# Kernel optimization log

Measured on AMD Instinct MI355X. Metric: run time of the kernel, lower is better.

Reference implementation:

```python
import jax, jax.numpy as jnp
import numpy as np

IN_FEATURES, OUT_FEATURES, KERNEL_DIMS = 1024, 128, 8
BATCH = 256


def setup_inputs() -> dict:
    key = jax.random.key(0)
    kx, kT = jax.random.split(key)
    x = jax.random.normal(kx, (BATCH, IN_FEATURES), dtype=jnp.float32)
    T = jax.random.normal(kT, (IN_FEATURES, OUT_FEATURES, KERNEL_DIMS), dtype=jnp.float32)
    return {"x": x, "T": T}


def reference(x, T):
    B = x.shape[0]
    in_f, out_f, kd = T.shape
    # M: (B, out_features, kernel_dims)
    M = (x @ T.reshape(in_f, out_f * kd)).reshape(B, out_f, kd)
    # pairwise L1 distance over kernel dims: (B, B, out_features)
    diffs = jnp.abs(M[None, :, :, :] - M[:, None, :, :]).sum(axis=3)
    # similarity features: sum over other samples, subtract self-term (exp(0)=1)
    c = jnp.exp(-diffs).sum(axis=1) - 1.0  # (B, out_features)
    return jnp.concatenate([x, c], axis=1)
```

## Files before the change

### kernel.cpp

```cpp
#include <hip/hip_runtime.h>
#include <stdint.h>

#define BATCH 256
#define INF   1024
#define OUTF  128
#define KD    8
#define NN    1024
#define OROW  1152

#define XCHW 2048
#define TCHW 2112

typedef __attribute__((ext_vector_type(8))) short short8;
typedef __attribute__((ext_vector_type(4))) float f32x4;

__device__ __forceinline__ unsigned short f2bf(float f) {
    union { float f; uint32_t u; } v; v.f = f;
    uint32_t r = v.u + 0x7FFFu + ((v.u >> 16) & 1u);
    return (unsigned short)(r >> 16);
}

__device__ __forceinline__ void stage_xt(
    const float* __restrict__ x, const float* __restrict__ T,
    float* xbuf, float* tbuf, int a0, int n0, int c, int wave, int lane)
{
    {
        const int r = lane >> 4, seg = lane & 15;
        #pragma unroll
        for (int p = 0; p < 2; ++p) {
            const int i = wave * 2 + p;
            const int row = i * 4 + r;
            const int segS = seg ^ (row & 7);
            const float* src = x + (size_t)(a0 + row) * INF + c * 64 + segS * 4;
            float* dst = xbuf + i * 256;
            __builtin_amdgcn_global_load_lds(
                (const __attribute__((address_space(1))) unsigned int*)src,
                (__attribute__((address_space(3))) unsigned int*)dst, 16, 0, 0);
        }
    }
    {
        const int kr = lane >> 3, seg = lane & 7;
        #pragma unroll
        for (int p = 0; p < 2; ++p) {
            const int i = wave * 2 + p;
            const int k = i * 8 + kr;
            const float* src = T + (size_t)(c * 64 + k) * NN + n0 + seg * 4;
            float* dst = tbuf + i * 264;
            __builtin_amdgcn_global_load_lds(
                (const __attribute__((address_space(1))) unsigned int*)src,
                (__attribute__((address_space(3))) unsigned int*)dst, 16, 0, 0);
        }
    }
}

__global__ __launch_bounds__(256, 2) void gemm_kernel(
    const float* __restrict__ x, const float* __restrict__ T,
    float* __restrict__ out)
{
    __shared__ __align__(16) float xls[3 * XCHW];
    __shared__ __align__(16) float tls[3 * TCHW];

    const int bid = blockIdx.x;
    const int a0 = (bid & 7) << 5;
    const int n0 = (bid >> 3) << 5;
    const int t = threadIdx.x, wave = t >> 6, lane = t & 63;
    const int rc = lane & 15, quad = lane >> 4;
    const int h = wave >> 1, g = wave & 1;
    const int rloc = h * 16 + rc;
    const int r7 = rc & 7;
    const int cn = g * 16 + rc;

    stage_xt(x, T, xls, tls, a0, n0, 0, wave, lane);
    stage_xt(x, T, xls + XCHW, tls + TCHW, a0, n0, 1, wave, lane);

    f32x4 acc = {0.f, 0.f, 0.f, 0.f};

    for (int c = 0; c < 16; ++c) {
        if (c == 15) { asm volatile("s_waitcnt vmcnt(0)" ::: "memory"); }
        else         { asm volatile("s_waitcnt vmcnt(4)" ::: "memory"); }
        __builtin_amdgcn_sched_barrier(0);
        __builtin_amdgcn_s_barrier();
        if (c + 2 < 16)
            stage_xt(x, T, xls + ((c + 2) % 3) * XCHW, tls + ((c + 2) % 3) * TCHW,
                     a0, n0, c + 2, wave, lane);
        const float* xc = xls + (c % 3) * XCHW;
        const float* tc = tls + (c % 3) * TCHW;
        #pragma unroll
        for (int ks = 0; ks < 2; ++ks) {
            f32x4 av0 = *(const f32x4*)(xc + rloc * 64 + (((ks * 8 + quad * 2 + 0) ^ r7) << 2));
            f32x4 av1 = *(const f32x4*)(xc + rloc * 64 + (((ks * 8 + quad * 2 + 1) ^ r7) << 2));
            float bv[8];
            #pragma unroll
            for (int j = 0; j < 8; ++j)
                bv[j] = tc[(ks * 4 + quad) * 264 + j * 32 + cn];
            short8 af, bf;
            af[0] = (short)f2bf(av0[0]); af[1] = (short)f2bf(av0[1]);
            af[2] = (short)f2bf(av0[2]); af[3] = (short)f2bf(av0[3]);
            af[4] = (short)f2bf(av1[0]); af[5] = (short)f2bf(av1[1]);
            af[6] = (short)f2bf(av1[2]); af[7] = (short)f2bf(av1[3]);
            #pragma unroll
            for (int j = 0; j < 8; ++j) bf[j] = (short)f2bf(bv[j]);
            acc = __builtin_amdgcn_mfma_f32_16x16x32_bf16(af, bf, acc, 0, 0, 0);
        }
    }

    #pragma unroll
    for (int r = 0; r < 4; ++r)
        out[(size_t)(a0 + h * 16 + quad * 4 + r) * OROW + (n0 + g * 16 + rc)] = acc[r];
}

__global__ __launch_bounds__(256, 4) void pair_kernel(
    const float* __restrict__ Msrc, float* __restrict__ out)
{
    __shared__ __align__(16) float Mloc[256 * 12];
    __shared__ float red[256];
    const int o = blockIdx.x >> 1;
    const int ha = blockIdx.x & 1;
    const int t = threadIdx.x;

    {
        const float* src = Msrc + (size_t)t * OROW + o * 8;
        f32x4 v0 = *(const f32x4*)(src);
        f32x4 v1 = *(const f32x4*)(src + 4);
        *(f32x4*)(Mloc + t * 12) = v0;
        *(f32x4*)(Mloc + t * 12 + 4) = v1;
    }
    __syncthreads();

    const int ai = t & 127, hb = t >> 7;
    const int a = ha * 128 + ai;
    f32x4 m0 = *(const f32x4*)(Mloc + a * 12);
    f32x4 m1 = *(const f32x4*)(Mloc + a * 12 + 4);
    float ssum = 0.f;
    #pragma unroll 4
    for (int j = 0; j < 128; ++j) {
        const float* mb = Mloc + (hb * 128 + j) * 12;
        f32x4 q0 = *(const f32x4*)(mb);
        f32x4 q1 = *(const f32x4*)(mb + 4);
        float d = fabsf(m0[0] - q0[0]) + fabsf(m0[1] - q0[1])
                + fabsf(m0[2] - q0[2]) + fabsf(m0[3] - q0[3])
                + fabsf(m1[0] - q1[0]) + fabsf(m1[1] - q1[1])
                + fabsf(m1[2] - q1[2]) + fabsf(m1[3] - q1[3]);
        ssum += __expf(-d);
    }
    red[t] = ssum;
    __syncthreads();
    if (t < 128)
        out[(size_t)(ha * 128 + t) * OROW + INF + o] = red[t] + red[t + 128] - 1.0f;
}

__global__ __launch_bounds__(256) void copy_kernel(
    const float* __restrict__ x, float* __restrict__ out)
{
    const int bx = blockIdx.x, t = threadIdx.x;
    #pragma unroll
    for (int p = 0; p < 4; ++p) {
        const int a = bx * 4 + p;
        const int j = t * 4;
        float4 v = *(const float4*)(x + (size_t)a * INF + j);
        *(float4*)(out + (size_t)a * OROW + j) = v;
    }
}

extern "C" void kernel_launch(void* const* d_in, const int* in_sizes, int n_in,
                              void* d_out, int out_size, void* d_ws, size_t ws_size,
                              hipStream_t stream) {
    const float* x = (const float*)d_in[0];
    const float* T = (const float*)d_in[1];
    float* out = (float*)d_out;
    (void)d_ws; (void)ws_size;

    gemm_kernel<<<256, 256, 0, stream>>>(x, T, out);
    pair_kernel<<<256, 256, 0, stream>>>(out, out);
    copy_kernel<<<64, 256, 0, stream>>>(x, out);
}
```

Before: 85.95 us.

## Deepen GEMM LDS pipeline, fuse copy into pair kernel, use workspace for M

The GEMM now uses a six-buffer LDS ring with five chunks in flight. Its inner step is written in inline asm that issues LDS reads and then a single lgkmcnt wait, uses hardware packed bf16 conversion, and splits the work across two accumulators. M goes to a separate workspace buffer, so the x copy no longer has to wait for the pair kernel, and the copy kernel is merged into the pair kernel, removing one launch. The pair kernel moves to 512 threads, splitting the inner loop four ways, and loads M into LDS with direct global-to-LDS loads. The risks are more LDS per block, which lowers occupancy, and hand-written waitcnt values that must match the number of loads in flight.

```diff
diff --git a/kernel.cpp b/kernel.cpp
--- a/kernel.cpp
+++ b/kernel.cpp
@@ -4,47 +4,56 @@
 #define BATCH 256
 #define INF   1024
 #define OUTF  128
-#define KD    8
 #define NN    1024
 #define OROW  1152
 
-#define XCHW 2048
-#define TCHW 2112
+#define XCH   2048
+#define TCH   2112
+#define NBUF  6
 
 typedef __attribute__((ext_vector_type(8))) short short8;
 typedef __attribute__((ext_vector_type(4))) float f32x4;
 
-__device__ __forceinline__ unsigned short f2bf(float f) {
-    union { float f; uint32_t u; } v; v.f = f;
-    uint32_t r = v.u + 0x7FFFu + ((v.u >> 16) & 1u);
-    return (unsigned short)(r >> 16);
+__device__ __forceinline__ short8 cvt8v(f32x4 lo, f32x4 hi) {
+    union { short8 s; uint32_t u[4]; } r;
+    asm("v_cvt_pk_bf16_f32 %0, %1, %2" : "=v"(r.u[0]) : "v"(lo[0]), "v"(lo[1]));
+    asm("v_cvt_pk_bf16_f32 %0, %1, %2" : "=v"(r.u[1]) : "v"(lo[2]), "v"(lo[3]));
+    asm("v_cvt_pk_bf16_f32 %0, %1, %2" : "=v"(r.u[2]) : "v"(hi[0]), "v"(hi[1]));
+    asm("v_cvt_pk_bf16_f32 %0, %1, %2" : "=v"(r.u[3]) : "v"(hi[2]), "v"(hi[3]));
+    return r.s;
+}
+__device__ __forceinline__ short8 cvt8s(float a, float b, float c, float d,
+                                        float e, float f, float g, float h) {
+    union { short8 s; uint32_t u[4]; } r;
+    asm("v_cvt_pk_bf16_f32 %0, %1, %2" : "=v"(r.u[0]) : "v"(a), "v"(b));
+    asm("v_cvt_pk_bf16_f32 %0, %1, %2" : "=v"(r.u[1]) : "v"(c), "v"(d));
+    asm("v_cvt_pk_bf16_f32 %0, %1, %2" : "=v"(r.u[2]) : "v"(e), "v"(f));
+    asm("v_cvt_pk_bf16_f32 %0, %1, %2" : "=v"(r.u[3]) : "v"(g), "v"(h));
+    return r.s;
 }
 
 __device__ __forceinline__ void stage_xt(
     const float* __restrict__ x, const float* __restrict__ T,
     float* xbuf, float* tbuf, int a0, int n0, int c, int wave, int lane)
 {
-    {
-        const int r = lane >> 4, seg = lane & 15;
+    {   const int r = lane >> 4, seg = lane & 15;
         #pragma unroll
         for (int p = 0; p < 2; ++p) {
             const int i = wave * 2 + p;
             const int row = i * 4 + r;
-            const int segS = seg ^ (row & 7);
-            const float* src = x + (size_t)(a0 + row) * INF + c * 64 + segS * 4;
+            const float* src = x + (size_t)(a0 + row) * INF + c * 64 + ((seg ^ (row & 7)) << 2);
             float* dst = xbuf + i * 256;
             __builtin_amdgcn_global_load_lds(
                 (const __attribute__((address_space(1))) unsigned int*)src,
                 (__attribute__((address_space(3))) unsigned int*)dst, 16, 0, 0);
         }
     }
-    {
-        const int kr = lane >> 3, seg = lane & 7;
+    {   const int kr = lane >> 3, seg = lane & 7;
         #pragma unroll
         for (int p = 0; p < 2; ++p) {
             const int i = wave * 2 + p;
             const int k = i * 8 + kr;
-            const float* src = T + (size_t)(c * 64 + k) * NN + n0 + seg * 4;
+            const float* src = T + (size_t)(c * 64 + k) * NN + n0 + (seg << 2);
             float* dst = tbuf + i * 264;
             __builtin_amdgcn_global_load_lds(
                 (const __attribute__((address_space(1))) unsigned int*)src,
@@ -53,90 +62,134 @@
     }
 }
 
-__global__ __launch_bounds__(256, 2) void gemm_kernel(
+#define GSTEP(c, VM) do {                                                     \
+    const uint32_t bb = xrow + (uint32_t)(((c) % NBUF) * (XCH * 4));          \
+    const uint32_t tb = tcol + (uint32_t)(((c) % NBUF) * (TCH * 4));          \
+    f32x4 av0, av1; float b0,b1,b2,b3,b4,b5,b6,b7;                            \
+    asm volatile(                                                             \
+        "s_waitcnt vmcnt(" #VM ")\n\t"                                        \
+        "s_barrier\n\t"                                                       \
+        "ds_read_b128 %0, %10\n\t"                                            \
+        "ds_read_b128 %1, %11\n\t"                                            \
+        "ds_read_b32 %2, %12\n\t"                                             \
+        "ds_read_b32 %3, %12 offset:128\n\t"                                  \
+        "ds_read_b32 %4, %12 offset:256\n\t"                                  \
+        "ds_read_b32 %5, %12 offset:384\n\t"                                  \
+        "ds_read_b32 %6, %12 offset:512\n\t"                                  \
+        "ds_read_b32 %7, %12 offset:640\n\t"                                  \
+        "ds_read_b32 %8, %12 offset:768\n\t"                                  \
+        "ds_read_b32 %9, %12 offset:896\n\t"                                  \
+        "s_waitcnt lgkmcnt(0)"                                                \
+        : "=&v"(av0), "=&v"(av1), "=&v"(b0), "=&v"(b1), "=&v"(b2), "=&v"(b3), \
+          "=&v"(b4), "=&v"(b5), "=&v"(b6), "=&v"(b7)                          \
+        : "v"(bb + gA00), "v"(bb + gA01), "v"(tb)                             \
+        : "memory");                                                          \
+    accA = __builtin_amdgcn_mfma_f32_16x16x32_bf16(                           \
+        cvt8v(av0, av1), cvt8s(b0,b1,b2,b3,b4,b5,b6,b7), accA, 0, 0, 0);      \
+    f32x4 av2, av3; float c0,c1,c2,c3,c4,c5,c6,c7;                            \
+    asm volatile(                                                             \
+        "ds_read_b128 %0, %10\n\t"                                            \
+        "ds_read_b128 %1, %11\n\t"                                            \
+        "ds_read_b32 %2, %12 offset:4224\n\t"                                 \
+        "ds_read_b32 %3, %12 offset:4352\n\t"                                 \
+        "ds_read_b32 %4, %12 offset:4480\n\t"                                 \
+        "ds_read_b32 %5, %12 offset:4608\n\t"                                 \
+        "ds_read_b32 %6, %12 offset:4736\n\t"                                 \
+        "ds_read_b32 %7, %12 offset:4864\n\t"                                 \
+        "ds_read_b32 %8, %12 offset:4992\n\t"                                 \
+        "ds_read_b32 %9, %12 offset:5120\n\t"                                 \
+        "s_waitcnt lgkmcnt(0)"                                                \
+        : "=&v"(av2), "=&v"(av3), "=&v"(c0), "=&v"(c1), "=&v"(c2), "=&v"(c3), \
+          "=&v"(c4), "=&v"(c5), "=&v"(c6), "=&v"(c7)                          \
+        : "v"(bb + gA10), "v"(bb + gA11), "v"(tb)                             \
+        : "memory");                                                          \
+    accB = __builtin_amdgcn_mfma_f32_16x16x32_bf16(                           \
+        cvt8v(av2, av3), cvt8s(c0,c1,c2,c3,c4,c5,c6,c7), accB, 0, 0, 0);      \
+} while (0)
+
+__global__ __launch_bounds__(256) void gemm_kernel(
     const float* __restrict__ x, const float* __restrict__ T,
-    float* __restrict__ out)
+    float* __restrict__ M)
 {
-    __shared__ __align__(16) float xls[3 * XCHW];
-    __shared__ __align__(16) float tls[3 * TCHW];
+    __shared__ __align__(16) float xls[NBUF * XCH];
+    __shared__ __align__(16) float tls[NBUF * TCH];
 
     const int bid = blockIdx.x;
     const int a0 = (bid & 7) << 5;
     const int n0 = (bid >> 3) << 5;
     const int t = threadIdx.x, wave = t >> 6, lane = t & 63;
-    const int rc = lane & 15, quad = lane >> 4;
+    const int rc = lane & 15, quad = lane >> 4, r7 = rc & 7;
     const int h = wave >> 1, g = wave & 1;
     const int rloc = h * 16 + rc;
-    const int r7 = rc & 7;
     const int cn = g * 16 + rc;
 
-    stage_xt(x, T, xls, tls, a0, n0, 0, wave, lane);
-    stage_xt(x, T, xls + XCHW, tls + TCHW, a0, n0, 1, wave, lane);
-
-    f32x4 acc = {0.f, 0.f, 0.f, 0.f};
-
-    for (int c = 0; c < 16; ++c) {
-        if (c == 15) { asm volatile("s_waitcnt vmcnt(0)" ::: "memory"); }
-        else         { asm volatile("s_waitcnt vmcnt(4)" ::: "memory"); }
-        __builtin_amdgcn_sched_barrier(0);
-        __builtin_amdgcn_s_barrier();
-        if (c + 2 < 16)
-            stage_xt(x, T, xls + ((c + 2) % 3) * XCHW, tls + ((c + 2) % 3) * TCHW,
-                     a0, n0, c + 2, wave, lane);
-        const float* xc = xls + (c % 3) * XCHW;
-        const float* tc = tls + (c % 3) * TCHW;
-        #pragma unroll
-        for (int ks = 0; ks < 2; ++ks) {
-            f32x4 av0 = *(const f32x4*)(xc + rloc * 64 + (((ks * 8 + quad * 2 + 0) ^ r7) << 2));
-            f32x4 av1 = *(const f32x4*)(xc + rloc * 64 + (((ks * 8 + quad * 2 + 1) ^ r7) << 2));
-            float bv[8];
-            #pragma unroll
-            for (int j = 0; j < 8; ++j)
-                bv[j] = tc[(ks * 4 + quad) * 264 + j * 32 + cn];
-            short8 af, bf;
-            af[0] = (short)f2bf(av0[0]); af[1] = (short)f2bf(av0[1]);
-            af[2] = (short)f2bf(av0[2]); af[3] = (short)f2bf(av0[3]);
-            af[4] = (short)f2bf(av1[0]); af[5] = (short)f2bf(av1[1]);
-            af[6] = (short)f2bf(av1[2]); af[7] = (short)f2bf(av1[3]);
-            #pragma unroll
-            for (int j = 0; j < 8; ++j) bf[j] = (short)f2bf(bv[j]);
-            acc = __builtin_amdgcn_mfma_f32_16x16x32_bf16(af, bf, acc, 0, 0, 0);
-        }
-    }
+    for (int c = 0; c < 5; ++c)
+        stage_xt(x, T, xls + c * XCH, tls + c * TCH, a0, n0, c, wave, lane);
+    asm volatile("s_waitcnt vmcnt(0)" ::: "memory");
+    __syncthreads();
+
+    f32x4 accA = {0.f, 0.f, 0.f, 0.f}, accB = {0.f, 0.f, 0.f, 0.f};
+    const uint32_t xrow = (uint32_t)(uintptr_t)(&xls[0]) + (uint32_t)(rloc * 256);
+    const uint32_t tcol = (uint32_t)(uintptr_t)(&tls[0]) + (uint32_t)((quad * 264 + cn) * 4);
+    const uint32_t gA00 = (uint32_t)(((quad * 2 + 0) ^ r7) << 4);
+    const uint32_t gA01 = (uint32_t)(((quad * 2 + 1) ^ r7) << 4);
+    const uint32_t gA10 = (uint32_t)(((8 + quad * 2 + 0) ^ r7) << 4);
+    const uint32_t gA11 = (uint32_t)(((8 + quad * 2 + 1) ^ r7) << 4);
+
+    for (int c = 0; c <= 10; ++c) {
+        GSTEP(c, 16);
+        stage_xt(x, T, xls + ((c + 5) % NBUF) * XCH, tls + ((c + 5) % NBUF) * TCH,
+                 a0, n0, c + 5, wave, lane);
+    }
+    GSTEP(11, 16);
+    GSTEP(12, 12);
+    GSTEP(13, 8);
+    GSTEP(14, 4);
+    GSTEP(15, 0);
 
     #pragma unroll
     for (int r = 0; r < 4; ++r)
-        out[(size_t)(a0 + h * 16 + quad * 4 + r) * OROW + (n0 + g * 16 + rc)] = acc[r];
-}
-
-__global__ __launch_bounds__(256, 4) void pair_kernel(
-    const float* __restrict__ Msrc, float* __restrict__ out)
+        M[(size_t)(a0 + h * 16 + quad * 4 + r) * NN + n0 + g * 16 + rc]
+            = accA[r] + accB[r];
+}
+
+__global__ __launch_bounds__(512) void pair_kernel(
+    const float* __restrict__ x, const float* __restrict__ M,
+    float* __restrict__ out)
 {
-    __shared__ __align__(16) float Mloc[256 * 12];
-    __shared__ float red[256];
-    const int o = blockIdx.x >> 1;
-    const int ha = blockIdx.x & 1;
-    const int t = threadIdx.x;
-
+    __shared__ __align__(16) float Mloc[256 * 8];
+    __shared__ float red[512];
+
+    const int bid = blockIdx.x;
+    const int o = bid >> 1, half = bid & 1;
+    const int t = threadIdx.x, wave = t >> 6, lane = t & 63;
+
+    if (t < 256) {
+        float4 v = *(const float4*)(x + (size_t)bid * INF + t * 4);
+        *(float4*)(out + (size_t)bid * OROW + t * 4) = v;
+    }
     {
-        const float* src = Msrc + (size_t)t * OROW + o * 8;
-        f32x4 v0 = *(const f32x4*)(src);
-        f32x4 v1 = *(const f32x4*)(src + 4);
-        *(f32x4*)(Mloc + t * 12) = v0;
-        *(f32x4*)(Mloc + t * 12 + 4) = v1;
-    }
+        const float* src = M + (size_t)(wave * 32 + (lane >> 1)) * NN
+                             + o * 8 + (lane & 1) * 4;
+        float* dst = Mloc + wave * 256;
+        __builtin_amdgcn_global_load_lds(
+            (const __attribute__((address_space(1))) unsigned int*)src,
+            (__attribute__((address_space(3))) unsigned int*)dst, 16, 0, 0);
+    }
+    asm volatile("s_waitcnt vmcnt(0)" ::: "memory");
     __syncthreads();
 
-    const int ai = t & 127, hb = t >> 7;
-    const int a = ha * 128 + ai;
-    f32x4 m0 = *(const f32x4*)(Mloc + a * 12);
-    f32x4 m1 = *(const f32x4*)(Mloc + a * 12 + 4);
+    const int ar = t & 127;
+    const int bq = t >> 7;
+    const int a = half * 128 + ar;
+    f32x4 m0 = *(const f32x4*)(Mloc + a * 8);
+    f32x4 m1 = *(const f32x4*)(Mloc + a * 8 + 4);
     float ssum = 0.f;
     #pragma unroll 4
-    for (int j = 0; j < 128; ++j) {
-        const float* mb = Mloc + (hb * 128 + j) * 12;
-        f32x4 q0 = *(const f32x4*)(mb);
-        f32x4 q1 = *(const f32x4*)(mb + 4);
+    for (int j = 0; j < 64; ++j) {
+        const float* qp = Mloc + (bq * 64 + j) * 8;
+        f32x4 q0 = *(const f32x4*)(qp);
+        f32x4 q1 = *(const f32x4*)(qp + 4);
         float d = fabsf(m0[0] - q0[0]) + fabsf(m0[1] - q0[1])
                 + fabsf(m0[2] - q0[2]) + fabsf(m0[3] - q0[3])
                 + fabsf(m1[0] - q1[0]) + fabsf(m1[1] - q1[1])
@@ -145,20 +198,9 @@
     }
     red[t] = ssum;
     __syncthreads();
-    if (t < 128)
-        out[(size_t)(ha * 128 + t) * OROW + INF + o] = red[t] + red[t + 128] - 1.0f;
-}
-
-__global__ __launch_bounds__(256) void copy_kernel(
-    const float* __restrict__ x, float* __restrict__ out)
-{
-    const int bx = blockIdx.x, t = threadIdx.x;
-    #pragma unroll
-    for (int p = 0; p < 4; ++p) {
-        const int a = bx * 4 + p;
-        const int j = t * 4;
-        float4 v = *(const float4*)(x + (size_t)a * INF + j);
-        *(float4*)(out + (size_t)a * OROW + j) = v;
+    if (t < 128) {
+        float s = red[t] + red[t + 128] + red[t + 256] + red[t + 384];
+        out[(size_t)(half * 128 + t) * OROW + INF + o] = s - 1.0f;
     }
 }
 
@@ -168,9 +210,8 @@
     const float* x = (const float*)d_in[0];
     const float* T = (const float*)d_in[1];
     float* out = (float*)d_out;
-    (void)d_ws; (void)ws_size;
-
-    gemm_kernel<<<256, 256, 0, stream>>>(x, T, out);
-    pair_kernel<<<256, 256, 0, stream>>>(out, out);
-    copy_kernel<<<64, 256, 0, stream>>>(x, out);
-}
+    float* M = (float*)d_ws;
+
+    gemm_kernel<<<256, 256, 0, stream>>>(x, T, M);
+    pair_kernel<<<256, 512, 0, stream>>>(x, M, out);
+}
```

After: 72.32 us. -15.9%, faster.
